# Kernel optimization log

Hardware: AMD Instinct MI355X
Metric: run time of the kernel (lower is better)

The kernel has to match this reference:

```python
import jax, jax.numpy as jnp
import numpy as np

H = 16        # attention heads
KVH = 4       # kv heads (GQA)
D = 128       # qk head_dim = qk_nope(64) + qk_rope(64)
ROPE = 64     # rotary sub-dim
VCH = 128     # v_channels
HID = 2048    # hidden size
E = 8         # routed experts
K = 2         # top-k
EPS = 1e-6
THETA = 10000.0


def rmsnorm(x, w):
    return x * jax.lax.rsqrt(jnp.mean(x * x, axis=-1, keepdims=True) + EPS) * w


def apply_rope(x, pos):
    # x: [T, h, ROPE]; rotate-half convention on the rope sub-dim
    half = ROPE // 2
    inv_freq = 1.0 / (THETA ** (jnp.arange(half, dtype=jnp.float32) / half))
    ang = pos.astype(jnp.float32)[:, None] * inv_freq          # [T, half]
    cos = jnp.cos(ang)[:, None, :]
    sin = jnp.sin(ang)[:, None, :]
    x1, x2 = x[..., :half], x[..., half:]
    return jnp.concatenate([x1 * cos - x2 * sin, x1 * sin + x2 * cos], axis=-1)


def swiglu(x, w_gate, w_up, w_down):
    return (jax.nn.silu(x @ w_gate) * (x @ w_up)) @ w_down


def setup_inputs() -> dict:
    key = jax.random.key(0)
    ks = jax.random.split(key, 16)
    T = 2048
    sc = 0.02
    n = lambda k, s: jax.random.normal(k, s, dtype=jnp.float32) * sc
    return {
        "x": jax.random.normal(ks[0], (T, HID), dtype=jnp.float32),
        "positions": jnp.arange(T, dtype=jnp.int32),
        "ln1_w": jnp.ones((HID,), jnp.float32),
        "qkv_w": n(ks[1], (HID, H * D + KVH * D + KVH * VCH)),
        "qkv_b": n(ks[2], (H * D + KVH * D + KVH * VCH,)),
        "k_ln_w": jnp.ones((D,), jnp.float32),
        "o_w": n(ks[3], (H * VCH, HID)),
        "ln2_w": jnp.ones((HID,), jnp.float32),
        "router_w": n(ks[4], (HID, E)),
        "w1": n(ks[5], (E, HID, 512)),
        "w2": n(ks[6], (E, 512, HID)),
        "w3": n(ks[7], (E, HID, 512)),
        "sw1": n(ks[8], (HID, 1024)),
        "sw2": n(ks[9], (1024, HID)),
        "sw3": n(ks[10], (HID, 1024)),
    }


def reference(x, positions, ln1_w, qkv_w, qkv_b, k_ln_w, o_w, ln2_w,
              router_w, w1, w2, w3, sw1, sw2, sw3):
    T = x.shape[0]
    # --- attention block ---
    h = rmsnorm(x, ln1_w)
    qkv = h @ qkv_w + qkv_b
    q = qkv[:, : H * D].reshape(T, H, D)
    k = qkv[:, H * D : H * D + KVH * D].reshape(T, KVH, D)
    v = qkv[:, H * D + KVH * D :].reshape(T, KVH, VCH)
    k = rmsnorm(k, k_ln_w)  # per-head k_layernorm over head_dim
    # rope applied to the trailing qk_rope_dim of q/k
    q = jnp.concatenate([q[..., : D - ROPE], apply_rope(q[..., D - ROPE :], positions)], -1)
    k = jnp.concatenate([k[..., : D - ROPE], apply_rope(k[..., D - ROPE :], positions)], -1)
    rep = H // KVH
    kf = jnp.repeat(k, rep, axis=1)   # [T, H, D]
    vf = jnp.repeat(v, rep, axis=1)   # [T, H, VCH]
    scale = D ** -0.5
    scores = jnp.einsum("qhd,khd->hqk", q, kf) * scale
    causal = jnp.tril(jnp.ones((T, T), dtype=bool))
    scores = jnp.where(causal[None], scores, jnp.float32(-1e30))
    p = jax.nn.softmax(scores, axis=-1)
    attn = jnp.einsum("hqk,khv->qhv", p, vf).reshape(T, H * VCH)
    x = x + attn @ o_w
    # --- MoE block: shared expert + top-k routed experts ---
    h2 = rmsnorm(x, ln2_w)
    probs = jax.nn.softmax(h2 @ router_w, axis=-1)            # [T, E]
    topw, topi = jax.lax.top_k(probs, K)
    topw = topw / jnp.sum(topw, axis=-1, keepdims=True)        # renormalize top-k
    combine = jnp.sum(jax.nn.one_hot(topi, E, dtype=h2.dtype) * topw[..., None], axis=1)  # [T, E]
    moe = swiglu(h2, sw1, sw3, sw2)                            # shared expert
    for e in range(E):  # small fixed expert count
        moe = moe + combine[:, e : e + 1] * swiglu(h2, w1[e], w3[e], w2[e])
    return x + moe
```

## Files before the change

### kernel.cpp

```cpp
#include <hip/hip_runtime.h>


typedef _Float16 half_t;
typedef _Float16 half8 __attribute__((ext_vector_type(8)));
typedef _Float16 half2v __attribute__((ext_vector_type(2)));
typedef float    f32x4 __attribute__((ext_vector_type(4)));
typedef float    floatx4 __attribute__((ext_vector_type(4)));

#define T_TOK 2048
#define HIDN  2048
#define NH    16
#define NKVH  4
#define HD    128
#define QKV_N 3072
#define NEXP  8
#define NPAIR_MAX 4608

#define MFMA16(a,b,c) __builtin_amdgcn_mfma_f32_16x16x32_f16(a,b,c,0,0,0)

__device__ __forceinline__ void gload_lds16(const half_t* g, half_t* l) {
    __builtin_amdgcn_global_load_lds(
        (const __attribute__((address_space(1))) void*)g,
        (__attribute__((address_space(3))) void*)l, 16, 0, 0);
}

__device__ __forceinline__ float silu_f(float g) {
    return g / (1.0f + expf(-g));
}

__global__ __launch_bounds__(256)
void rmsnorm_split_k(const float* __restrict__ x, const float* __restrict__ w,
                     half_t* __restrict__ hi, half_t* __restrict__ lo)
{
    const int row = blockIdx.x, tid = threadIdx.x;
    const float* xr = x + (size_t)row * HIDN;
    floatx4 v0 = *(const floatx4*)(xr + tid * 8);
    floatx4 v1 = *(const floatx4*)(xr + tid * 8 + 4);
    float ss = v0[0]*v0[0] + v0[1]*v0[1] + v0[2]*v0[2] + v0[3]*v0[3]
             + v1[0]*v1[0] + v1[1]*v1[1] + v1[2]*v1[2] + v1[3]*v1[3];
    for (int o = 32; o; o >>= 1) ss += __shfl_down(ss, o);
    __shared__ float red[4];
    if ((tid & 63) == 0) red[tid >> 6] = ss;
    __syncthreads();
    ss = red[0] + red[1] + red[2] + red[3];
    float rs = rsqrtf(ss * (1.0f / HIDN) + 1e-6f);
    floatx4 w0 = *(const floatx4*)(w + tid * 8);
    floatx4 w1 = *(const floatx4*)(w + tid * 8 + 4);
    float vv[8] = { v0[0]*w0[0], v0[1]*w0[1], v0[2]*w0[2], v0[3]*w0[3],
                    v1[0]*w1[0], v1[1]*w1[1], v1[2]*w1[2], v1[3]*w1[3] };
    half8 hv, lv;
#pragma unroll
    for (int j = 0; j < 8; ++j) {
        float o = vv[j] * rs;
        half_t h = (half_t)o;
        hv[j] = h;
        lv[j] = (half_t)((o - (float)h) * 1024.0f);
    }
    *(half8*)(hi + (size_t)row * HIDN + tid * 8) = hv;
    if (lo) *(half8*)(lo + (size_t)row * HIDN + tid * 8) = lv;
}

__global__ __launch_bounds__(256)
void transpose_split2(const float* __restrict__ src,
                      half_t* __restrict__ dh, half_t* __restrict__ dl,
                      int sstride, int dstride)
{
    __shared__ float tile[32][36];
    const int n0 = blockIdx.x * 32, k0 = blockIdx.y * 32;
    const int tid = threadIdx.x;
    {
        int r = tid >> 3, c = (tid & 7) * 4;
        *(floatx4*)&tile[r][c] =
            *(const floatx4*)(src + (size_t)(k0 + r) * sstride + n0 + c);
    }
    __syncthreads();
    int n = tid & 31, g = tid >> 5, gg = g & 3;
    half8 hv;
    if (g < 4) {
#pragma unroll
        for (int j = 0; j < 8; ++j) hv[j] = (half_t)tile[gg * 8 + j][n];
        *(half8*)(dh + (size_t)(n0 + n) * dstride + k0 + gg * 8) = hv;
    } else {
#pragma unroll
        for (int j = 0; j < 8; ++j) {
            float v = tile[gg * 8 + j][n];
            half_t h = (half_t)v;
            hv[j] = (half_t)((v - (float)h) * 1024.0f);
        }
        *(half8*)(dl + (size_t)(n0 + n) * dstride + k0 + gg * 8) = hv;
    }
}

__global__ __launch_bounds__(256)
void transpose_f16(const float* __restrict__ src, half_t* __restrict__ dh,
                   int sstride, int dstride)
{
    __shared__ float tile[32][68];
    const int n0 = blockIdx.x * 64, k0 = blockIdx.y * 32;
    const int tid = threadIdx.x;
    {
        int r = tid >> 3, c = (tid & 7) * 4;
        const float* s = src + (size_t)(k0 + r) * sstride + n0;
        *(floatx4*)&tile[r][c]      = *(const floatx4*)(s + c);
        *(floatx4*)&tile[r][c + 32] = *(const floatx4*)(s + c + 32);
    }
    __syncthreads();
    int n = tid & 63, g = tid >> 6;
    half8 hv;
#pragma unroll
    for (int j = 0; j < 8; ++j) hv[j] = (half_t)tile[g * 8 + j][n];
    *(half8*)(dh + (size_t)(n0 + n) * dstride + k0 + g * 8) = hv;
}

__global__ __launch_bounds__(256)
void vt_transpose_perm(const float* __restrict__ src, half_t* __restrict__ dh)
{
    __shared__ float tile[32][68];
    const int n0 = blockIdx.x * 64, k0 = blockIdx.y * 32;
    const int tid = threadIdx.x;
    {
        int r = tid >> 3, c = (tid & 7) * 4;
        const float* s = src + (size_t)(k0 + r) * QKV_N + n0;
        *(floatx4*)&tile[r][c]      = *(const floatx4*)(s + c);
        *(floatx4*)&tile[r][c + 32] = *(const floatx4*)(s + c + 32);
    }
    __syncthreads();
    int n = tid & 63, g = tid >> 6;
    half8 hv;
#pragma unroll
    for (int tt = 0; tt < 8; ++tt) {
        int c_src = (tt & 1) * 16 + 4 * g + (tt >> 1);
        hv[tt] = (half_t)tile[c_src][n];
    }
    *(half8*)(dh + (size_t)(n0 + n) * T_TOK + k0 + g * 8) = hv;
}

__global__ __launch_bounds__(256)
void w13_transpose(const float* __restrict__ sw1, const float* __restrict__ w1,
                   const float* __restrict__ sw3, const float* __restrict__ w3,
                   half_t* __restrict__ dst)
{
    __shared__ float tile[32][68];
    const int n0 = blockIdx.x * 64, k0 = blockIdx.y * 32;
    const int tid = threadIdx.x;
    const float* base;
    int stride;
    if (n0 < 1024)      { base = sw1 + n0; stride = 1024; }
    else if (n0 < 2048) { base = sw3 + (n0 - 1024); stride = 1024; }
    else if (n0 < 6144) { int e = (n0 - 2048) >> 9;
                          base = w1 + (size_t)e * HIDN * 512 + ((n0 - 2048) & 511);
                          stride = 512; }
    else                { int e = (n0 - 6144) >> 9;
                          base = w3 + (size_t)e * HIDN * 512 + ((n0 - 6144) & 511);
                          stride = 512; }
    {
        int r = tid >> 3, c = (tid & 7) * 4;
        const float* s = base + (size_t)(k0 + r) * stride;
        *(floatx4*)&tile[r][c]      = *(const floatx4*)(s + c);
        *(floatx4*)&tile[r][c + 32] = *(const floatx4*)(s + c + 32);
    }
    __syncthreads();
    int n = tid & 63, g = tid >> 6;
    half8 hv;
#pragma unroll
    for (int j = 0; j < 8; ++j) hv[j] = (half_t)tile[g * 8 + j][n];
    *(half8*)(dst + (size_t)(n0 + n) * HIDN + k0 + g * 8) = hv;
}

__global__ __launch_bounds__(256)
void w2_transpose(const float* __restrict__ sw2, const float* __restrict__ w2,
                  half_t* __restrict__ dst)
{
    __shared__ float tile[32][68];
    const int n0 = blockIdx.x * 64, k0 = blockIdx.y * 32;
    const int tid = threadIdx.x;
    {
        int r = tid >> 3, c = (tid & 7) * 4;
        int k = k0 + r;
        const float* s;
        if (k < 1024) s = sw2 + (size_t)k * HIDN + n0;
        else {
            int e = (k - 1024) >> 9, kk = (k - 1024) & 511;
            s = w2 + ((size_t)e * 512 + kk) * HIDN + n0;
        }
        *(floatx4*)&tile[r][c]      = *(const floatx4*)(s + c);
        *(floatx4*)&tile[r][c + 32] = *(const floatx4*)(s + c + 32);
    }
    __syncthreads();
    int n = tid & 63, g = tid >> 6;
    half8 hv;
#pragma unroll
    for (int j = 0; j < 8; ++j) hv[j] = (half_t)tile[g * 8 + j][n];
    *(half8*)(dst + (size_t)(n0 + n) * 5120 + k0 + g * 8) = hv;
}

__global__ __launch_bounds__(256)
void owu_kernel(const float* __restrict__ ow, const float* __restrict__ ln2w,
                const float* __restrict__ rw, float* __restrict__ owu,
                int* __restrict__ cnt, int* __restrict__ pairTok,
                float* __restrict__ pairW)
{
    if (blockIdx.x < 18) {
        int idx = blockIdx.x * 256 + threadIdx.x;
        if (idx < NPAIR_MAX) { pairTok[idx] = 0; pairW[idx] = 0.0f; }
        if (idx < NEXP) cnt[idx] = 0;
    }
    const int k = blockIdx.x * 4 + (threadIdx.x >> 6);
    const int lane = threadIdx.x & 63;
    float acc[NEXP] = {};
    const float* row = ow + (size_t)k * HIDN;
#pragma unroll
    for (int j = 0; j < 8; ++j) {
        int c = j * 256 + lane * 4;
        floatx4 ov = *(const floatx4*)(row + c);
        floatx4 lw = *(const floatx4*)(ln2w + c);
#pragma unroll
        for (int i = 0; i < 4; ++i) {
            float s = ov[i] * lw[i];
            const float* rwc = rw + (size_t)(c + i) * NEXP;
#pragma unroll
            for (int e = 0; e < NEXP; ++e) acc[e] += s * rwc[e];
        }
    }
#pragma unroll
    for (int e = 0; e < NEXP; ++e)
        for (int o = 32; o; o >>= 1) acc[e] += __shfl_down(acc[e], o);
    if (lane == 0) {
#pragma unroll
        for (int e = 0; e < NEXP; ++e) owu[(size_t)k * NEXP + e] = acc[e];
    }
}

__global__ __launch_bounds__(256)
void z_kernel(const float* __restrict__ qkv, const float* __restrict__ owu,
              float* __restrict__ zbuf)
{
    const int kv = blockIdx.x, tid = threadIdx.x;
    const int hh = tid >> 4, li = tid & 15;
    const float* vrow = qkv + (size_t)kv * QKV_N + 2560 + (hh >> 2) * HD;
    const int d0 = li * 8;
    float acc[NEXP] = {};
#pragma unroll
    for (int j = 0; j < 8; ++j) {
        float v = vrow[d0 + j];
        const float* ou = owu + (size_t)(hh * HD + d0 + j) * NEXP;
#pragma unroll
        for (int e = 0; e < NEXP; ++e) acc[e] += v * ou[e];
    }
#pragma unroll
    for (int e = 0; e < NEXP; ++e)
        for (int o = 1; o < 16; o <<= 1) acc[e] += __shfl_xor(acc[e], o);
    if (li == 0) {
#pragma unroll
        for (int e = 0; e < NEXP; ++e)
            zbuf[((size_t)hh * T_TOK + kv) * NEXP + e] = acc[e];
    }
}

template<bool SPLIT, int BM>
__global__ __launch_bounds__(256, 2)
void gemm_f16(const half_t* __restrict__ Ah, const half_t* __restrict__ Al,
              const half_t* __restrict__ Bth, const half_t* __restrict__ Btl,
              const float* __restrict__ bias, const float* __restrict__ res,
              float* __restrict__ Cf, half_t* __restrict__ Ch,
              int M, int N, int K, int lda, int ldb)
{
    constexpr int NBUF = SPLIT ? 2 : 1;
    constexpr int MR = BM / 32;
    __shared__ half_t As[2][NBUF][BM * 32];
    __shared__ half_t Bs[2][NBUF][128 * 32];
    const int tid = threadIdx.x, lane = tid & 63, wid = tid >> 6;
    const int l15 = lane & 15, l4 = lane >> 4;
    const int row0 = blockIdx.y * BM, col0 = blockIdx.x * 128;
    const int wr = (wid >> 1) * (BM / 2), wc = (wid & 1) * 64;
    f32x4 accM[MR][4] = {}, accC[MR][4] = {};
    const int lrw = lane >> 2, lcl = (lane & 3) * 8;

#define STAGE(BUF, K0)                                                        \
    do {                                                                      \
        _Pragma("unroll")                                                     \
        for (int j = 0; j < BM / 64; ++j) {                                   \
            const int r = wid * (BM / 4) + j * 16;                            \
            const size_t ga = (size_t)(row0 + r + lrw) * lda + (K0) + lcl;    \
            gload_lds16(Ah + ga, &As[BUF][0][r * 32]);                        \
            if constexpr (SPLIT) gload_lds16(Al + ga, &As[BUF][1][r * 32]);   \
        }                                                                     \
        _Pragma("unroll")                                                     \
        for (int j = 0; j < 2; ++j) {                                         \
            const int r = wid * 32 + j * 16;                                  \
            const size_t gb = (size_t)(col0 + r + lrw) * ldb + (K0) + lcl;    \
            gload_lds16(Bth + gb, &Bs[BUF][0][r * 32]);                       \
            if constexpr (SPLIT) gload_lds16(Btl + gb, &Bs[BUF][1][r * 32]);  \
        }                                                                     \
    } while (0)

    STAGE(0, 0);
    __syncthreads();
    int cur = 0;
    for (int k0 = 0; k0 < K; k0 += 32, cur ^= 1) {
        if (k0 + 32 < K) STAGE(cur ^ 1, k0 + 32);
        half8 ah[MR], al[MR], bh[4], bl[4];
#pragma unroll
        for (int m = 0; m < MR; ++m) {
            int off = (wr + m * 16 + l15) * 32 + l4 * 8;
            ah[m] = *(const half8*)&As[cur][0][off];
            if constexpr (SPLIT) al[m] = *(const half8*)&As[cur][1][off];
        }
#pragma unroll
        for (int n = 0; n < 4; ++n) {
            int off = (wc + n * 16 + l15) * 32 + l4 * 8;
            bh[n] = *(const half8*)&Bs[cur][0][off];
            if constexpr (SPLIT) bl[n] = *(const half8*)&Bs[cur][1][off];
        }
#pragma unroll
        for (int m = 0; m < MR; ++m)
#pragma unroll
            for (int n = 0; n < 4; ++n) {
                accM[m][n] = MFMA16(ah[m], bh[n], accM[m][n]);
                if constexpr (SPLIT) {
                    accC[m][n] = MFMA16(ah[m], bl[n], accC[m][n]);
                    accC[m][n] = MFMA16(al[m], bh[n], accC[m][n]);
                }
            }
        __syncthreads();
    }
#undef STAGE

#pragma unroll
    for (int m = 0; m < MR; ++m) {
#pragma unroll
        for (int n = 0; n < 4; ++n) {
            int gr0 = row0 + wr + m * 16 + l4 * 4;
            int gc  = col0 + wc + n * 16 + l15;
            float b = bias ? bias[gc] : 0.0f;
#pragma unroll
            for (int i = 0; i < 4; ++i) {
                float v = accM[m][n][i];
                if constexpr (SPLIT) v += accC[m][n][i] * (1.0f / 1024.0f);
                v += b;
                size_t idx = (size_t)(gr0 + i) * N + gc;
                if (res) v += res[idx];
                if (Cf) Cf[idx] = v;
                if (Ch) Ch[idx] = (half_t)v;
            }
        }
    }
}

__global__ __launch_bounds__(256, 2)
void gemm_gu_all(const half_t* __restrict__ h2, const half_t* __restrict__ W13t,
                 const int* __restrict__ pairTok, const int* __restrict__ basep,
                 const float* __restrict__ pairW,
                 half_t* __restrict__ As_out, half_t* __restrict__ Ab_out)
{
    __shared__ half_t As[2][64 * 32];
    __shared__ half_t Bs[2][128 * 32];
    __shared__ half_t ex[64][136];
    const int bid = blockIdx.x;
    const bool grouped = (bid >= 512);
    int ct, row0;
    if (!grouped) { ct = bid & 15;          row0 = (bid >> 4) * 64; }
    else          { int g = bid - 512; ct = g & 7; row0 = (g >> 3) * 64; }
    const int tid = threadIdx.x, lane = tid & 63, wid = tid >> 6;
    const int l15 = lane & 15, l4 = lane >> 4;
    const int lrw = lane >> 2, lcl = (lane & 3) * 8;
    int gbase, ubase;
    if (grouped) {
        int e = 0;
#pragma unroll
        for (int i = 1; i < NEXP; ++i) if (row0 >= basep[i]) e = i;
        gbase = 2048 + 512 * e + ct * 64;
        ubase = 6144 + 512 * e + ct * 64;
    } else {
        gbase = ct * 64;
        ubase = 1024 + ct * 64;
    }
    const int wr = (wid >> 1) * 32, wc = (wid & 1) * 64;
    const half_t* Abase;
    if (grouped) {
        const int tok = pairTok[row0 + wid * 16 + lrw];
        Abase = h2 + (size_t)tok * HIDN + lcl;
    } else {
        Abase = h2 + (size_t)(row0 + wid * 16 + lrw) * HIDN + lcl;
    }
    f32x4 acc[2][4] = {};

#define GSTAGE(BUF, K0)                                                       \
    do {                                                                      \
        gload_lds16(Abase + (K0), &As[BUF][(wid * 16) * 32]);                 \
        _Pragma("unroll")                                                     \
        for (int j = 0; j < 2; ++j) {                                         \
            const int r = wid * 32 + j * 16;                                  \
            const int grow = (r < 64) ? gbase + r : ubase + (r - 64);         \
            const size_t gb = (size_t)(grow + lrw) * HIDN + (K0) + lcl;       \
            gload_lds16(W13t + gb, &Bs[BUF][r * 32]);                         \
        }                                                                     \
    } while (0)

    GSTAGE(0, 0);
    __syncthreads();
    int cur = 0;
    for (int k0 = 0; k0 < HIDN; k0 += 32, cur ^= 1) {
        if (k0 + 32 < HIDN) GSTAGE(cur ^ 1, k0 + 32);
        half8 ah[2], bh[4];
#pragma unroll
        for (int m = 0; m < 2; ++m)
            ah[m] = *(const half8*)&As[cur][(wr + m * 16 + l15) * 32 + l4 * 8];
#pragma unroll
        for (int n = 0; n < 4; ++n)
            bh[n] = *(const half8*)&Bs[cur][(wc + n * 16 + l15) * 32 + l4 * 8];
#pragma unroll
        for (int m = 0; m < 2; ++m)
#pragma unroll
            for (int n = 0; n < 4; ++n)
                acc[m][n] = MFMA16(ah[m], bh[n], acc[m][n]);
        __syncthreads();
    }
#undef GSTAGE

#pragma unroll
    for (int m = 0; m < 2; ++m)
#pragma unroll
        for (int n = 0; n < 4; ++n)
#pragma unroll
            for (int i = 0; i < 4; ++i)
                ex[wr + m * 16 + l4 * 4 + i][wc + n * 16 + l15] =
                    (half_t)acc[m][n][i];
    __syncthreads();
    const int OSTR = grouped ? 512 : 1024;
    half_t* outp = grouped ? Ab_out : As_out;
#pragma unroll
    for (int w2 = 0; w2 < 2; ++w2) {
        int unit = tid * 2 + w2;
        int row = unit >> 3, cgx = (unit & 7) * 8;
        half8 g8 = *(const half8*)&ex[row][cgx];
        half8 u8 = *(const half8*)&ex[row][64 + cgx];
        float wgt = grouped ? pairW[row0 + row] : 1.0f;
        half8 o8;
#pragma unroll
        for (int j = 0; j < 8; ++j)
            o8[j] = (half_t)(silu_f((float)g8[j]) * (float)u8[j] * wgt);
        *(half8*)(outp + (size_t)(row0 + row) * OSTR + ct * 64 + cgx) = o8;
    }
}

__global__ __launch_bounds__(256, 2)
void gemm_down_all(const half_t* __restrict__ As_sh, const half_t* __restrict__ Ab,
                   const half_t* __restrict__ W2t, const int* __restrict__ basep,
                   const float* __restrict__ x2, float* __restrict__ out,
                   half_t* __restrict__ Ypair)
{
    __shared__ half_t Asm[2][64 * 32];
    __shared__ half_t Bsm[2][128 * 32];
    const int tid = threadIdx.x, lane = tid & 63, wid = tid >> 6;
    const int l15 = lane & 15, l4 = lane >> 4;
    const int lrw = lane >> 2, lcl = (lane & 3) * 8;
    const int col0 = blockIdx.x * 128;
    const bool shared = (blockIdx.y < 32);
    const int row0 = (shared ? blockIdx.y : blockIdx.y - 32) * 64;
    const half_t* A;
    int lda, K, bcol;
    if (shared) { A = As_sh; lda = 1024; K = 1024; bcol = 0; }
    else {
        int e = 0;
#pragma unroll
        for (int i = 1; i < NEXP; ++i) if (row0 >= basep[i]) e = i;
        A = Ab; lda = 512; K = 512; bcol = 1024 + 512 * e;
    }
    const int wr = (wid >> 1) * 32, wc = (wid & 1) * 64;
    f32x4 acc[2][4] = {};

#define DSTAGE(BUF, K0)                                                       \
    do {                                                                      \
        const size_t ga = (size_t)(row0 + wid * 16 + lrw) * lda + (K0) + lcl; \
        gload_lds16(A + ga, &Asm[BUF][(wid * 16) * 32]);                      \
        _Pragma("unroll")                                                     \
        for (int j = 0; j < 2; ++j) {                                         \
            const int r = wid * 32 + j * 16;                                  \
            const size_t gb = (size_t)(col0 + r + lrw) * 5120 + bcol + (K0) + lcl; \
            gload_lds16(W2t + gb, &Bsm[BUF][r * 32]);                         \
        }                                                                     \
    } while (0)

    DSTAGE(0, 0);
    __syncthreads();
    int cur = 0;
    for (int k0 = 0; k0 < K; k0 += 32, cur ^= 1) {
        if (k0 + 32 < K) DSTAGE(cur ^ 1, k0 + 32);
        half8 ah[2], bh[4];
#pragma unroll
        for (int m = 0; m < 2; ++m)
            ah[m] = *(const half8*)&Asm[cur][(wr + m * 16 + l15) * 32 + l4 * 8];
#pragma unroll
        for (int n = 0; n < 4; ++n)
            bh[n] = *(const half8*)&Bsm[cur][(wc + n * 16 + l15) * 32 + l4 * 8];
#pragma unroll
        for (int m = 0; m < 2; ++m)
#pragma unroll
            for (int n = 0; n < 4; ++n)
                acc[m][n] = MFMA16(ah[m], bh[n], acc[m][n]);
        __syncthreads();
    }
#undef DSTAGE

#pragma unroll
    for (int m = 0; m < 2; ++m)
#pragma unroll
        for (int n = 0; n < 4; ++n) {
            int gr0 = row0 + wr + m * 16 + l4 * 4;
            int gc  = col0 + wc + n * 16 + l15;
#pragma unroll
            for (int i = 0; i < 4; ++i) {
                size_t idx = (size_t)(gr0 + i) * HIDN + gc;
                if (shared) out[idx] = x2[idx] + acc[m][n][i];
                else        Ypair[idx] = (half_t)acc[m][n][i];
            }
        }
}

__global__ __launch_bounds__(256)
void qkv_prep(const float* __restrict__ qkv, const int* __restrict__ pos,
              const float* __restrict__ klnw,
              half_t* __restrict__ qh, half_t* __restrict__ ql,
              half_t* __restrict__ kh, half_t* __restrict__ kl)
{
    const int t = blockIdx.x, tid = threadIdx.x, lane = tid & 63, wid = tid >> 6;
    const float* row = qkv + (size_t)t * QKV_N;
    __shared__ float cs[32], sn[32];
    if (tid < 32) {
        double freq = exp((double)tid * -0.28782313662425572);
        double ang = (double)pos[t] * freq;
        const double twopi = 6.283185307179586476925286766559;
        ang -= twopi * floor(ang * (1.0 / twopi));
        float a = (float)ang;
        cs[tid] = cosf(a);
        sn[tid] = sinf(a);
    }
    __syncthreads();

    const float qscale = 0.08838834764831845f;
    {
        const int hh = tid >> 4, d0 = (tid & 15) * 8;
        const float* qrow = row + hh * HD;
        float outv[8];
        if (d0 < 64) {
#pragma unroll
            for (int j = 0; j < 8; ++j) outv[j] = qrow[d0 + j];
        } else if (d0 < 96) {
            int j0 = d0 - 64;
#pragma unroll
            for (int j = 0; j < 8; ++j) {
                int jj = j0 + j;
                outv[j] = qrow[64 + jj] * cs[jj] - qrow[96 + jj] * sn[jj];
            }
        } else {
            int j0 = d0 - 96;
#pragma unroll
            for (int j = 0; j < 8; ++j) {
                int jj = j0 + j;
                outv[j] = qrow[64 + jj] * sn[jj] + qrow[96 + jj] * cs[jj];
            }
        }
        half8 hv, lv;
#pragma unroll
        for (int j = 0; j < 8; ++j) {
            float o = outv[j] * qscale;
            half_t h = (half_t)o;
            hv[j] = h;
            lv[j] = (half_t)((o - (float)h) * 1024.0f);
        }
        size_t base = (size_t)t * (NH * HD) + hh * HD + d0;
        *(half8*)(qh + base) = hv;
        *(half8*)(ql + base) = lv;
    }
    {
        const float* krow = row + NH * HD + wid * HD;
        float a0 = krow[lane], a1 = krow[64 + lane];
        float ss = a0 * a0 + a1 * a1;
        for (int o = 32; o; o >>= 1) ss += __shfl_down(ss, o);
        ss = __shfl(ss, 0);
        float rs = rsqrtf(ss * (1.0f / HD) + 1e-6f);
        float n0 = a0 * rs * klnw[lane];
        float n1 = a1 * rs * klnw[64 + lane];
        float other = __shfl_xor(n1, 32);
        int j = lane & 31;
        float o1 = (lane < 32) ? (n1 * cs[j] - other * sn[j])
                               : (other * sn[j] + n1 * cs[j]);
        size_t base = (size_t)t * (NKVH * HD) + wid * HD;
        half_t h;
        h = (half_t)n0; kh[base + lane] = h;
        kl[base + lane] = (half_t)((n0 - (float)h) * 1024.0f);
        h = (half_t)o1; kh[base + 64 + lane] = h;
        kl[base + 64 + lane] = (half_t)((o1 - (float)h) * 1024.0f);
    }
}

__global__ __launch_bounds__(256, 2)
void attn_kernel(const half_t* __restrict__ qh, const half_t* __restrict__ ql,
                 const half_t* __restrict__ kh, const half_t* __restrict__ kl,
                 const half_t* __restrict__ vth, const float* __restrict__ zbuf,
                 half_t* __restrict__ oh,
                 float* __restrict__ Op0, float* __restrict__ Op1,
                 float* __restrict__ Op2, float* __restrict__ ml,
                 float* __restrict__ zpart, float* __restrict__ zfin)
{
    const int bid = blockIdx.x;
    const int h = bid & 15;
    int rrem = bid >> 4, q = 31, nch = 6, c = 0;
    for (; q >= 0; --q) {
        nch = (q + 6) / 6;
        if (rrem < nch) { c = rrem; break; }
        rrem -= nch;
    }
    const int nt = q + 1;
    const int kvbeg = ((c * nt) / nch) * 64;
    const int kvend = (((c + 1) * nt) / nch) * 64;

    const int kvh = h >> 2;
    const int tid = threadIdx.x, lane = tid & 63, wid = tid >> 6;
    const int q0 = q * 64 + wid * 16;
    const int l15 = lane & 15, l4 = lane >> 4;

    __shared__ half_t Ksh[64][136], Ksl[64][136];
    __shared__ half_t Vsh[128][72];
    __shared__ half_t Ph[4][16][72];
    __shared__ float  zsh[64][8];

    half8 qfh[4], qfl[4];
    {
        const size_t qb = (size_t)(q0 + l15) * (NH * HD) + h * HD + l4 * 8;
#pragma unroll
        for (int cc = 0; cc < 4; ++cc) {
            qfh[cc] = *(const half8*)(qh + qb + cc * 32);
            qfl[cc] = *(const half8*)(ql + qb + cc * 32);
        }
    }

    f32x4 om[8] = {};
    f32x4 zacA[4] = {}, zacB[4] = {};
    float mrow[4] = { -1e30f, -1e30f, -1e30f, -1e30f };
    float lrow[4] = {};

    const int kr = tid >> 2, kc0 = (tid & 3) * 32;
    const int vd = tid >> 1, vc0 = (tid & 1) * 32;
    const int zr = tid >> 3, zc = tid & 7;
    uint4 rkh0, rkh1, rkh2, rkh3, rkl0, rkl1, rkl2, rkl3;
    uint4 rv0, rv1, rv2, rv3;
    float rz0, rz1;

#define LOAD_TILE(KV0)                                                        \
    do {                                                                      \
        size_t sk = (size_t)((KV0) + kr) * (NKVH * HD) + kvh * HD + kc0;      \
        rkh0 = *(const uint4*)(kh + sk);       rkl0 = *(const uint4*)(kl + sk);      \
        rkh1 = *(const uint4*)(kh + sk + 8);   rkl1 = *(const uint4*)(kl + sk + 8);  \
        rkh2 = *(const uint4*)(kh + sk + 16);  rkl2 = *(const uint4*)(kl + sk + 16); \
        rkh3 = *(const uint4*)(kh + sk + 24);  rkl3 = *(const uint4*)(kl + sk + 24); \
        size_t sv = (size_t)(kvh * HD + vd) * T_TOK + (KV0) + vc0;            \
        rv0 = *(const uint4*)(vth + sv);       rv1 = *(const uint4*)(vth + sv + 8);  \
        rv2 = *(const uint4*)(vth + sv + 16);  rv3 = *(const uint4*)(vth + sv + 24); \
        rz0 = zbuf[((size_t)h * T_TOK + (KV0) + zr) * 8 + zc];                \
        rz1 = zbuf[((size_t)h * T_TOK + (KV0) + 32 + zr) * 8 + zc];           \
    } while (0)

    LOAD_TILE(kvbeg);
    for (int kv0 = kvbeg; kv0 < kvend; kv0 += 64) {
        *(uint4*)&Ksh[kr][kc0]      = rkh0;  *(uint4*)&Ksl[kr][kc0]      = rkl0;
        *(uint4*)&Ksh[kr][kc0 + 8]  = rkh1;  *(uint4*)&Ksl[kr][kc0 + 8]  = rkl1;
        *(uint4*)&Ksh[kr][kc0 + 16] = rkh2;  *(uint4*)&Ksl[kr][kc0 + 16] = rkl2;
        *(uint4*)&Ksh[kr][kc0 + 24] = rkh3;  *(uint4*)&Ksl[kr][kc0 + 24] = rkl3;
        *(uint4*)&Vsh[vd][vc0]      = rv0;   *(uint4*)&Vsh[vd][vc0 + 8]  = rv1;
        *(uint4*)&Vsh[vd][vc0 + 16] = rv2;   *(uint4*)&Vsh[vd][vc0 + 24] = rv3;
        zsh[zr][zc]      = rz0;
        zsh[32 + zr][zc] = rz1;
        __syncthreads();
        if (kv0 + 64 < kvend) LOAD_TILE(kv0 + 64);

        f32x4 sf[4];
        __builtin_amdgcn_s_setprio(1);
#pragma unroll
        for (int t2 = 0; t2 < 4; ++t2) {
            f32x4 s = {}, sc1 = {}, sc2 = {};
#pragma unroll
            for (int cc = 0; cc < 4; ++cc) {
                half8 bh = *(const half8*)&Ksh[t2 * 16 + l15][cc * 32 + l4 * 8];
                half8 bl = *(const half8*)&Ksl[t2 * 16 + l15][cc * 32 + l4 * 8];
                s   = MFMA16(qfh[cc], bh, s);
                sc1 = MFMA16(qfh[cc], bl, sc1);
                sc2 = MFMA16(qfl[cc], bh, sc2);
            }
            sf[t2] = s + (sc1 + sc2) * (1.0f / 1024.0f);
        }
        __builtin_amdgcn_s_setprio(0);

        float pmax[4];
#pragma unroll
        for (int i = 0; i < 4; ++i) {
            const int qg = q0 + l4 * 4 + i;
#pragma unroll
            for (int t2 = 0; t2 < 4; ++t2) {
                int kvg = kv0 + t2 * 16 + l15;
                if (kvg > qg) sf[t2][i] = -1e30f;
            }
            float mx = fmaxf(fmaxf(sf[0][i], sf[1][i]),
                             fmaxf(sf[2][i], sf[3][i]));
#pragma unroll
            for (int o = 1; o < 16; o <<= 1) mx = fmaxf(mx, __shfl_xor(mx, o));
            pmax[i] = mx;
        }
        float dm = fmaxf(fmaxf(pmax[0] - mrow[0], pmax[1] - mrow[1]),
                         fmaxf(pmax[2] - mrow[2], pmax[3] - mrow[3]));
        if (__any(dm > 6.0f)) {
#pragma unroll
            for (int i = 0; i < 4; ++i) {
                float mnew = fmaxf(mrow[i], pmax[i]);
                float resc = expf(mrow[i] - mnew);
                lrow[i] *= resc;
                zacA[i] *= resc;  zacB[i] *= resc;
#pragma unroll
                for (int c8 = 0; c8 < 8; ++c8) om[c8][i] *= resc;
                mrow[i] = mnew;
            }
        }
        f32x4 zt0a = *(const f32x4*)&zsh[l15][0];
        f32x4 zt0b = *(const f32x4*)&zsh[l15][4];
        f32x4 zt1a = *(const f32x4*)&zsh[16 + l15][0];
        f32x4 zt1b = *(const f32x4*)&zsh[16 + l15][4];
        f32x4 zt2a = *(const f32x4*)&zsh[32 + l15][0];
        f32x4 zt2b = *(const f32x4*)&zsh[32 + l15][4];
        f32x4 zt3a = *(const f32x4*)&zsh[48 + l15][0];
        f32x4 zt3b = *(const f32x4*)&zsh[48 + l15][4];
#pragma unroll
        for (int i = 0; i < 4; ++i) {
            float p0 = expf(sf[0][i] - mrow[i]);
            float p1 = expf(sf[1][i] - mrow[i]);
            float p2 = expf(sf[2][i] - mrow[i]);
            float p3 = expf(sf[3][i] - mrow[i]);
            lrow[i] += (p0 + p1) + (p2 + p3);
            zacA[i] += p0 * zt0a + p1 * zt1a + p2 * zt2a + p3 * zt3a;
            zacB[i] += p0 * zt0b + p1 * zt1b + p2 * zt2b + p3 * zt3b;
            half2v ppA = { (half_t)p0, (half_t)p1 };
            half2v ppB = { (half_t)p2, (half_t)p3 };
            *(half2v*)&Ph[wid][l4 * 4 + i][l15 * 2]      = ppA;
            *(half2v*)&Ph[wid][l4 * 4 + i][32 + l15 * 2] = ppB;
        }

        half8 pa0 = *(const half8*)&Ph[wid][l15][l4 * 8];
        half8 pa1 = *(const half8*)&Ph[wid][l15][32 + l4 * 8];
        __builtin_amdgcn_s_setprio(1);
#pragma unroll
        for (int c8 = 0; c8 < 8; ++c8) {
            half8 v0 = *(const half8*)&Vsh[c8 * 16 + l15][l4 * 8];
            half8 v1 = *(const half8*)&Vsh[c8 * 16 + l15][32 + l4 * 8];
            om[c8] = MFMA16(pa0, v0, om[c8]);
            om[c8] = MFMA16(pa1, v1, om[c8]);
        }
        __builtin_amdgcn_s_setprio(0);
        __syncthreads();
    }
#undef LOAD_TILE

#pragma unroll
    for (int i = 0; i < 4; ++i)
#pragma unroll
        for (int o = 1; o < 16; o <<= 1) lrow[i] += __shfl_xor(lrow[i], o);

    for (int o = 1; o < 16; o <<= 1) {
#pragma unroll
        for (int i = 0; i < 4; ++i)
#pragma unroll
            for (int k = 0; k < 4; ++k) {
                zacA[i][k] += __shfl_xor(zacA[i][k], o);
                zacB[i][k] += __shfl_xor(zacB[i][k], o);
            }
    }
    if (l15 == 0) {
#pragma unroll
        for (int i = 0; i < 4; ++i) {
            int row64 = wid * 16 + l4 * 4 + i;
            if (nch == 1) {
                float invl = 1.0f / lrow[i];
                size_t zo = ((size_t)(q * 64 + row64) * 16 + h) * 8;
                *(f32x4*)&zfin[zo]     = zacA[i] * invl;
                *(f32x4*)&zfin[zo + 4] = zacB[i] * invl;
            } else {
                size_t zo = ((size_t)bid * 64 + row64) * 8;
                *(f32x4*)&zpart[zo]     = zacA[i];
                *(f32x4*)&zpart[zo + 4] = zacB[i];
            }
        }
    }

    if (nch == 1) {
#pragma unroll
        for (int c8 = 0; c8 < 8; ++c8) {
#pragma unroll
            for (int i = 0; i < 4; ++i) {
                float v = om[c8][i] / lrow[i];
                size_t idx = (size_t)(q0 + l4 * 4 + i) * (NH * HD) + h * HD
                           + c8 * 16 + l15;
                oh[idx] = (half_t)v;
            }
        }
    } else {
        float* Op = (bid < 768)  ? Op0 + (size_t)bid * 8192
                  : (bid < 1280) ? Op1 + (size_t)(bid - 768) * 8192
                                 : Op2 + (size_t)(bid - 1280) * 8192;
#pragma unroll
        for (int c8 = 0; c8 < 8; ++c8) {
#pragma unroll
            for (int i = 0; i < 4; ++i) {
                int row64 = wid * 16 + l4 * 4 + i;
                Op[row64 * 128 + c8 * 16 + l15] = om[c8][i];
            }
        }
        if (l15 == 0) {
#pragma unroll
            for (int i = 0; i < 4; ++i) {
                int row64 = wid * 16 + l4 * 4 + i;
                ml[(size_t)bid * 128 + row64]      = mrow[i];
                ml[(size_t)bid * 128 + 64 + row64] = lrow[i];
            }
        }
    }
}

__device__ __forceinline__ const float* slot_ptr(int s, const float* Op0,
                                                 const float* Op1,
                                                 const float* Op2)
{
    return (s < 768)  ? Op0 + (size_t)s * 8192
         : (s < 1280) ? Op1 + (size_t)(s - 768) * 8192
                      : Op2 + (size_t)(s - 1280) * 8192;
}

__global__ __launch_bounds__(256)
void attn_combine(const float* __restrict__ Op0, const float* __restrict__ Op1,
                  const float* __restrict__ Op2, const float* __restrict__ ml,
                  const float* __restrict__ zpart,
                  half_t* __restrict__ oh, float* __restrict__ zfin)
{
    const int bid = blockIdx.x;
    const int h = bid & 15, q = 6 + (bid >> 4);
    const int nch = (q + 6) / 6;
    int r0 = 0;
    for (int j = 31; j > q; --j) r0 += (j + 6) / 6;
    const int tid = threadIdx.x;
    const int row = tid >> 2, cg = (tid & 3) * 32;

    float M = -1e30f;
    for (int c = 0; c < nch; ++c) {
        int s = (r0 + c) * 16 + h;
        M = fmaxf(M, ml[(size_t)s * 128 + row]);
    }
    float wsum = 0.0f;
    for (int c = 0; c < nch; ++c) {
        int s = (r0 + c) * 16 + h;
        wsum += ml[(size_t)s * 128 + 64 + row] *
                expf(ml[(size_t)s * 128 + row] - M);
    }
    float inv = 1.0f / wsum;

    if ((tid & 3) == 0) {
        f32x4 a = {0,0,0,0}, b = {0,0,0,0};
        for (int c = 0; c < nch; ++c) {
            int s = (r0 + c) * 16 + h;
            float w = expf(ml[(size_t)s * 128 + row] - M) * inv;
            size_t zo = ((size_t)s * 64 + row) * 8;
            a += w * (*(const f32x4*)&zpart[zo]);
            b += w * (*(const f32x4*)&zpart[zo + 4]);
        }
        size_t zo = ((size_t)(q * 64 + row) * 16 + h) * 8;
        *(f32x4*)&zfin[zo]     = a;
        *(f32x4*)&zfin[zo + 4] = b;
    }

    size_t obase = (size_t)(q * 64 + row) * (NH * HD) + h * HD + cg;
#pragma unroll
    for (int jj = 0; jj < 4; ++jj) {
        floatx4 a0 = {0,0,0,0}, a1 = {0,0,0,0};
        for (int c = 0; c < nch; ++c) {
            int s = (r0 + c) * 16 + h;
            float w = expf(ml[(size_t)s * 128 + row] - M) * inv;
            const float* base = slot_ptr(s, Op0, Op1, Op2) + row * 128 + cg;
            a0 += w * (*(const floatx4*)(base + jj * 8));
            a1 += w * (*(const floatx4*)(base + jj * 8 + 4));
        }
        half8 hv;
#pragma unroll
        for (int k = 0; k < 4; ++k) {
            hv[k]     = (half_t)a0[k];
            hv[4 + k] = (half_t)a1[k];
        }
        *(half8*)(oh + obase + jj * 8) = hv;
    }
}

__global__ __launch_bounds__(256)
void router_linear(const float* __restrict__ x, const float* __restrict__ zfin,
                   const float* __restrict__ x2,
                   const float* __restrict__ ln2w, const float* __restrict__ rw,
                   int* __restrict__ topi, float* __restrict__ topv,
                   int* __restrict__ cnt, half_t* __restrict__ h2)
{
    const int t = blockIdx.x, tid = threadIdx.x;
    const float* xr2 = x2 + (size_t)t * HIDN + tid * 8;
    floatx4 x2a = *(const floatx4*)(xr2);
    floatx4 x2b = *(const floatx4*)(xr2 + 4);
    float ss = x2a[0]*x2a[0] + x2a[1]*x2a[1] + x2a[2]*x2a[2] + x2a[3]*x2a[3]
             + x2b[0]*x2b[0] + x2b[1]*x2b[1] + x2b[2]*x2b[2] + x2b[3]*x2b[3];
    for (int o = 32; o; o >>= 1) ss += __shfl_down(ss, o);
    __shared__ float red[4];
    if ((tid & 63) == 0) red[tid >> 6] = ss;
    __syncthreads();
    ss = red[0] + red[1] + red[2] + red[3];
    float rs = rsqrtf(ss * (1.0f / HIDN) + 1e-6f);

    const float* xr = x + (size_t)t * HIDN + tid * 8;
    floatx4 xa = *(const floatx4*)(xr);
    floatx4 xb = *(const floatx4*)(xr + 4);
    floatx4 lwa = *(const floatx4*)(ln2w + tid * 8);
    floatx4 lwb = *(const floatx4*)(ln2w + tid * 8 + 4);

    float acc[NEXP] = {};
#pragma unroll
    for (int j = 0; j < 8; ++j) {
        int c = tid * 8 + j;
        float xv = (j < 4 ? xa[j] : xb[j - 4]) * (j < 4 ? lwa[j] : lwb[j - 4]);
        const float* rwc = rw + (size_t)c * NEXP;
#pragma unroll
        for (int e = 0; e < NEXP; ++e) acc[e] += xv * rwc[e];
    }
#pragma unroll
    for (int e = 0; e < NEXP; ++e)
        for (int o = 32; o; o >>= 1) acc[e] += __shfl_down(acc[e], o);
    __shared__ float red8[4][NEXP];
    if ((tid & 63) == 0)
#pragma unroll
        for (int e = 0; e < NEXP; ++e) red8[tid >> 6][e] = acc[e];

    __shared__ float zred[NEXP * 16];
    if (tid < 128) {
        int hh = tid >> 3, e = tid & 7;
        zred[e * 16 + hh] = zfin[((size_t)t * 16 + hh) * 8 + e];
    }

    half8 h2v;
#pragma unroll
    for (int j = 0; j < 8; ++j) {
        float xv = (j < 4 ? x2a[j] : x2b[j - 4]) * (j < 4 ? lwa[j] : lwb[j - 4]);
        h2v[j] = (half_t)(xv * rs);
    }
    *(half8*)(h2 + (size_t)t * HIDN + tid * 8) = h2v;

    __syncthreads();
    if (tid == 0) {
        float lg[NEXP];
#pragma unroll
        for (int e = 0; e < NEXP; ++e) {
            float zs = 0.0f;
#pragma unroll
            for (int hh = 0; hh < 16; ++hh) zs += zred[e * 16 + hh];
            lg[e] = (red8[0][e] + red8[1][e] + red8[2][e] + red8[3][e] + zs) * rs;
        }
        int i1 = 0;
        for (int e = 1; e < NEXP; ++e) if (lg[e] > lg[i1]) i1 = e;
        int i2 = (i1 == 0) ? 1 : 0;
        for (int e = 0; e < NEXP; ++e) if (e != i1 && lg[e] > lg[i2]) i2 = e;
        float mx = lg[i1];
        float p1 = expf(lg[i1] - mx), p2 = expf(lg[i2] - mx);
        float inv = 1.0f / (p1 + p2);
        topi[2 * t] = i1;       topi[2 * t + 1] = i2;
        topv[2 * t] = p1 * inv; topv[2 * t + 1] = p2 * inv;
        atomicAdd(&cnt[i1], 1);
        atomicAdd(&cnt[i2], 1);
    }
}

__global__ __launch_bounds__(256)
void moe_build(const int* __restrict__ cnt, int* __restrict__ basep,
               const int* __restrict__ topi, const float* __restrict__ topv,
               int* __restrict__ pairTok, float* __restrict__ pairW,
               int* __restrict__ pairPos)
{
    const int e = blockIdx.x;
    int base = 0;
    for (int i = 0; i < e; ++i) base += (cnt[i] + 63) & ~63;
    if (threadIdx.x == 0) basep[e] = base;

    const int tid = threadIdx.x, lane = tid & 63, wv = tid >> 6;
    __shared__ int wsum[4];
    int run = base;
    for (int i0 = 0; i0 < 2 * T_TOK; i0 += 256) {
        int i = i0 + tid;
        bool m = (topi[i] == e);
        unsigned long long bal = __ballot(m);
        int lpre = __popcll(bal & ((1ull << lane) - 1ull));
        if (lane == 0) wsum[wv] = (int)__popcll(bal);
        __syncthreads();
        int woff = 0;
        for (int w = 0; w < wv; ++w) woff += wsum[w];
        if (m) {
            int pos = run + woff + lpre;
            pairTok[pos] = i >> 1;
            pairW[pos]   = topv[i];
            pairPos[i]   = pos;
        }
        run += wsum[0] + wsum[1] + wsum[2] + wsum[3];
        __syncthreads();
    }
}

__global__ __launch_bounds__(256)
void moe_final(const half_t* __restrict__ Ypair, const int* __restrict__ pairPos,
               float* __restrict__ out)
{
    int t = blockIdx.x, c0 = threadIdx.x * 8;
    int p1 = pairPos[2 * t], p2 = pairPos[2 * t + 1];
    half8 y1 = *(const half8*)(Ypair + (size_t)p1 * HIDN + c0);
    half8 y2 = *(const half8*)(Ypair + (size_t)p2 * HIDN + c0);
    float* o = out + (size_t)t * HIDN + c0;
    floatx4 a = *(floatx4*)o, b = *(floatx4*)(o + 4);
#pragma unroll
    for (int j = 0; j < 4; ++j) {
        a[j] += (float)y1[j] + (float)y2[j];
        b[j] += (float)y1[4 + j] + (float)y2[4 + j];
    }
    *(floatx4*)o = a;
    *(floatx4*)(o + 4) = b;
}

extern "C" void kernel_launch(void* const* d_in, const int* in_sizes, int n_in,
                              void* d_out, int out_size, void* d_ws, size_t ws_size,
                              hipStream_t stream)
{
    (void)in_sizes; (void)n_in; (void)out_size; (void)ws_size;
    const float* x    = (const float*)d_in[0];
    const int*   pos  = (const int*)  d_in[1];
    const float* ln1w = (const float*)d_in[2];
    const float* qkvw = (const float*)d_in[3];
    const float* qkvb = (const float*)d_in[4];
    const float* klnw = (const float*)d_in[5];
    const float* ow   = (const float*)d_in[6];
    const float* ln2w = (const float*)d_in[7];
    const float* rw   = (const float*)d_in[8];
    const float* w1   = (const float*)d_in[9];
    const float* w2   = (const float*)d_in[10];
    const float* w3   = (const float*)d_in[11];
    const float* sw1  = (const float*)d_in[12];
    const float* sw2  = (const float*)d_in[13];
    const float* sw3  = (const float*)d_in[14];
    float* out = (float*)d_out;

    char* ws = (char*)d_ws;
    const size_t AB = 16842752;
    float*  x2      = (float*)(ws);
    half_t* h_hi    = (half_t*)(ws + AB);
    half_t* h_lo    = (half_t*)(ws + AB + 8388608);
    half_t* qkvwt_h = (half_t*)(ws + AB + 16777216);
    half_t* qkvwt_l = (half_t*)(ws + AB + 29360128);
    float*  qkv     = (float*)(ws + AB + 41943040);
    half_t* q_h     = (half_t*)(ws + AB + 67108864);
    half_t* q_l     = (half_t*)(ws + AB + 75497472);
    half_t* k_h     = (half_t*)(ws + AB + 83886080);
    half_t* k_l     = (half_t*)(ws + AB + 85983232);
    half_t* vt_h    = (half_t*)(ws + AB + 88080384);
    half_t* attn_h  = (half_t*)(ws + AB);
    float*  zbuf    = (float*)(ws + AB + 8388608);
    half_t* owt     = (half_t*)(ws + AB + 16777216);
    float*  ow_u    = (float*)(ws + AB + 25165824);
    float*  mlpart  = (float*)(ws + AB + 25231360);
    float*  Opart0  = (float*)(ws + AB + 41943040);
    float*  Opart1  = (float*)(ws);
    float*  Opart2  = (float*)(ws + AB + 29360128);
    half_t* h2      = (half_t*)(ws + AB + 33554432);
    half_t* W13t    = (half_t*)(ws + AB + 41943040);
    half_t* As_sh   = (half_t*)(ws + AB);
    half_t* Ab      = (half_t*)(ws + AB + 16777216);
    half_t* W2t     = (half_t*)(ws + AB + 41943040);
    half_t* Ypair   = (half_t*)(ws + AB + 92274688);

    char* meta = ws + (size_t)(AB + 117440512);
    int*    cnt     = (int*)  (meta + 0);
    int*    basep   = (int*)  (meta + 128);
    int*    topi    = (int*)  (meta + 256);
    float*  topv    = (float*)(meta + 16640);
    int*    pairPos = (int*)  (meta + 33024);
    int*    pairTok = (int*)  (meta + 49408);
    float*  pairW   = (float*)(meta + 67840);
    float*  zpart   = (float*)(meta + 131072);
    float*  zfin    = (float*)(meta + 131072 + 3342336);

    dim3 b256(256);

    rmsnorm_split_k<<<T_TOK, b256, 0, stream>>>(x, ln1w, h_hi, h_lo);
    transpose_split2<<<dim3(QKV_N / 32, HIDN / 32), b256, 0, stream>>>(
        qkvw, qkvwt_h, qkvwt_l, QKV_N, HIDN);
    gemm_f16<true, 64><<<dim3(QKV_N / 128, T_TOK / 64), b256, 0, stream>>>(
        h_hi, h_lo, qkvwt_h, qkvwt_l, qkvb, nullptr, qkv, nullptr,
        T_TOK, QKV_N, HIDN, HIDN, HIDN);
    qkv_prep<<<T_TOK, b256, 0, stream>>>(qkv, pos, klnw, q_h, q_l, k_h, k_l);
    vt_transpose_perm<<<dim3(512 / 64, T_TOK / 32), b256, 0, stream>>>(
        qkv + 2560, vt_h);
    transpose_f16<<<dim3(HIDN / 64, HIDN / 32), b256, 0, stream>>>(
        ow, owt, HIDN, HIDN);
    owu_kernel<<<512, b256, 0, stream>>>(ow, ln2w, rw, ow_u,
                                         cnt, pairTok, pairW);
    z_kernel<<<T_TOK, b256, 0, stream>>>(qkv, ow_u, zbuf);
    attn_kernel<<<1632, b256, 0, stream>>>(
        q_h, q_l, k_h, k_l, vt_h, zbuf, attn_h,
        Opart0, Opart1, Opart2, mlpart, zpart, zfin);
    attn_combine<<<416, b256, 0, stream>>>(Opart0, Opart1, Opart2, mlpart,
                                           zpart, attn_h, zfin);
    gemm_f16<false, 64><<<dim3(HIDN / 128, T_TOK / 64), b256, 0, stream>>>(
        attn_h, nullptr, owt, nullptr, nullptr, x, x2, nullptr,
        T_TOK, HIDN, HIDN, HIDN, HIDN);
    router_linear<<<T_TOK, b256, 0, stream>>>(
        x, zfin, x2, ln2w, rw, topi, topv, cnt, h2);
    moe_build<<<NEXP, b256, 0, stream>>>(cnt, basep, topi, topv,
                                         pairTok, pairW, pairPos);
    w13_transpose<<<dim3(10240 / 64, HIDN / 32), b256, 0, stream>>>(
        sw1, w1, sw3, w3, W13t);
    gemm_gu_all<<<512 + 8 * (NPAIR_MAX / 64), b256, 0, stream>>>(
        h2, W13t, pairTok, basep, pairW, As_sh, Ab);
    w2_transpose<<<dim3(HIDN / 64, 5120 / 32), b256, 0, stream>>>(sw2, w2, W2t);
    gemm_down_all<<<dim3(16, 104), b256, 0, stream>>>(
        As_sh, Ab, W2t, basep, x2, out, Ypair);
    moe_final<<<T_TOK, b256, 0, stream>>>(Ypair, pairPos, out);
}
```

Baseline: 614.2 us.

## Fold router z-accumulation into the PV MFMA as a ninth value tile

The per-head router projection z (8 experts) used to be accumulated in the attention kernel with scalar FMAs on fp32 values plus a cross-lane shuffle reduction. Now z is stored transposed and in fp16, in a permuted layout matching the P·V operand. It is appended to the V shared tile as 16 extra rows so one more MFMA per kv tile produces it. This removes the VALU accumulation and the shuffle reduction, at the cost of fp16 precision for z and of P also being fp16 in that product, which may affect router logits and top-k selection.

```diff
diff --git a/kernel.cpp b/kernel.cpp
--- a/kernel.cpp
+++ b/kernel.cpp
@@ -233,7 +233,7 @@
 
 __global__ __launch_bounds__(256)
 void z_kernel(const float* __restrict__ qkv, const float* __restrict__ owu,
-              float* __restrict__ zbuf)
+              half_t* __restrict__ zt)
 {
     const int kv = blockIdx.x, tid = threadIdx.x;
     const int hh = tid >> 4, li = tid & 15;
@@ -251,9 +251,12 @@
     for (int e = 0; e < NEXP; ++e)
         for (int o = 1; o < 16; o <<= 1) acc[e] += __shfl_xor(acc[e], o);
     if (li == 0) {
+        int j = kv & 31;
+        int s = ((j & 15) << 1) | (j >> 4);
+        size_t base = (size_t)(kv & ~31) + s;
 #pragma unroll
         for (int e = 0; e < NEXP; ++e)
-            zbuf[((size_t)hh * T_TOK + kv) * NEXP + e] = acc[e];
+            zt[(size_t)(hh * 8 + e) * T_TOK + base] = (half_t)acc[e];
     }
 }
 
@@ -598,7 +601,7 @@
 __global__ __launch_bounds__(256, 2)
 void attn_kernel(const half_t* __restrict__ qh, const half_t* __restrict__ ql,
                  const half_t* __restrict__ kh, const half_t* __restrict__ kl,
-                 const half_t* __restrict__ vth, const float* __restrict__ zbuf,
+                 const half_t* __restrict__ vth, const half_t* __restrict__ zt,
                  half_t* __restrict__ oh,
                  float* __restrict__ Op0, float* __restrict__ Op1,
                  float* __restrict__ Op2, float* __restrict__ ml,
@@ -622,9 +625,8 @@
     const int l15 = lane & 15, l4 = lane >> 4;
 
     __shared__ half_t Ksh[64][136], Ksl[64][136];
-    __shared__ half_t Vsh[128][72];
+    __shared__ half_t Vsh[144][72];
     __shared__ half_t Ph[4][16][72];
-    __shared__ float  zsh[64][8];
 
     half8 qfh[4], qfl[4];
     {
@@ -636,17 +638,16 @@
         }
     }
 
-    f32x4 om[8] = {};
-    f32x4 zacA[4] = {}, zacB[4] = {};
+    f32x4 om[9] = {};
     float mrow[4] = { -1e30f, -1e30f, -1e30f, -1e30f };
     float lrow[4] = {};
 
     const int kr = tid >> 2, kc0 = (tid & 3) * 32;
     const int vd = tid >> 1, vc0 = (tid & 1) * 32;
-    const int zr = tid >> 3, zc = tid & 7;
+    const int ze = tid >> 5, zc0 = (tid & 31) * 2;
     uint4 rkh0, rkh1, rkh2, rkh3, rkl0, rkl1, rkl2, rkl3;
     uint4 rv0, rv1, rv2, rv3;
-    float rz0, rz1;
+    unsigned rzw;
 
 #define LOAD_TILE(KV0)                                                        \
     do {                                                                      \
@@ -658,8 +659,7 @@
         size_t sv = (size_t)(kvh * HD + vd) * T_TOK + (KV0) + vc0;            \
         rv0 = *(const uint4*)(vth + sv);       rv1 = *(const uint4*)(vth + sv + 8);  \
         rv2 = *(const uint4*)(vth + sv + 16);  rv3 = *(const uint4*)(vth + sv + 24); \
-        rz0 = zbuf[((size_t)h * T_TOK + (KV0) + zr) * 8 + zc];                \
-        rz1 = zbuf[((size_t)h * T_TOK + (KV0) + 32 + zr) * 8 + zc];           \
+        rzw = *(const unsigned*)(zt + (size_t)(h * 8 + ze) * T_TOK + (KV0) + zc0);   \
     } while (0)
 
     LOAD_TILE(kvbeg);
@@ -670,8 +670,7 @@
         *(uint4*)&Ksh[kr][kc0 + 24] = rkh3;  *(uint4*)&Ksl[kr][kc0 + 24] = rkl3;
         *(uint4*)&Vsh[vd][vc0]      = rv0;   *(uint4*)&Vsh[vd][vc0 + 8]  = rv1;
         *(uint4*)&Vsh[vd][vc0 + 16] = rv2;   *(uint4*)&Vsh[vd][vc0 + 24] = rv3;
-        zsh[zr][zc]      = rz0;
-        zsh[32 + zr][zc] = rz1;
+        *(unsigned*)&Vsh[128 + ze][zc0] = rzw;
         __syncthreads();
         if (kv0 + 64 < kvend) LOAD_TILE(kv0 + 64);
 
@@ -715,20 +714,11 @@
                 float mnew = fmaxf(mrow[i], pmax[i]);
                 float resc = expf(mrow[i] - mnew);
                 lrow[i] *= resc;
-                zacA[i] *= resc;  zacB[i] *= resc;
-#pragma unroll
-                for (int c8 = 0; c8 < 8; ++c8) om[c8][i] *= resc;
+#pragma unroll
+                for (int c8 = 0; c8 < 9; ++c8) om[c8][i] *= resc;
                 mrow[i] = mnew;
             }
         }
-        f32x4 zt0a = *(const f32x4*)&zsh[l15][0];
-        f32x4 zt0b = *(const f32x4*)&zsh[l15][4];
-        f32x4 zt1a = *(const f32x4*)&zsh[16 + l15][0];
-        f32x4 zt1b = *(const f32x4*)&zsh[16 + l15][4];
-        f32x4 zt2a = *(const f32x4*)&zsh[32 + l15][0];
-        f32x4 zt2b = *(const f32x4*)&zsh[32 + l15][4];
-        f32x4 zt3a = *(const f32x4*)&zsh[48 + l15][0];
-        f32x4 zt3b = *(const f32x4*)&zsh[48 + l15][4];
 #pragma unroll
         for (int i = 0; i < 4; ++i) {
             float p0 = expf(sf[0][i] - mrow[i]);
@@ -736,8 +726,6 @@
             float p2 = expf(sf[2][i] - mrow[i]);
             float p3 = expf(sf[3][i] - mrow[i]);
             lrow[i] += (p0 + p1) + (p2 + p3);
-            zacA[i] += p0 * zt0a + p1 * zt1a + p2 * zt2a + p3 * zt3a;
-            zacB[i] += p0 * zt0b + p1 * zt1b + p2 * zt2b + p3 * zt3b;
             half2v ppA = { (half_t)p0, (half_t)p1 };
             half2v ppB = { (half_t)p2, (half_t)p3 };
             *(half2v*)&Ph[wid][l4 * 4 + i][l15 * 2]      = ppA;
@@ -748,7 +736,7 @@
         half8 pa1 = *(const half8*)&Ph[wid][l15][32 + l4 * 8];
         __builtin_amdgcn_s_setprio(1);
 #pragma unroll
-        for (int c8 = 0; c8 < 8; ++c8) {
+        for (int c8 = 0; c8 < 9; ++c8) {
             half8 v0 = *(const half8*)&Vsh[c8 * 16 + l15][l4 * 8];
             half8 v1 = *(const half8*)&Vsh[c8 * 16 + l15][32 + l4 * 8];
             om[c8] = MFMA16(pa0, v0, om[c8]);
@@ -764,28 +752,16 @@
 #pragma unroll
         for (int o = 1; o < 16; o <<= 1) lrow[i] += __shfl_xor(lrow[i], o);
 
-    for (int o = 1; o < 16; o <<= 1) {
-#pragma unroll
-        for (int i = 0; i < 4; ++i)
-#pragma unroll
-            for (int k = 0; k < 4; ++k) {
-                zacA[i][k] += __shfl_xor(zacA[i][k], o);
-                zacB[i][k] += __shfl_xor(zacB[i][k], o);
-            }
-    }
-    if (l15 == 0) {
+    if (l15 < 8) {
+        const int e = l15;
 #pragma unroll
         for (int i = 0; i < 4; ++i) {
             int row64 = wid * 16 + l4 * 4 + i;
             if (nch == 1) {
-                float invl = 1.0f / lrow[i];
-                size_t zo = ((size_t)(q * 64 + row64) * 16 + h) * 8;
-                *(f32x4*)&zfin[zo]     = zacA[i] * invl;
-                *(f32x4*)&zfin[zo + 4] = zacB[i] * invl;
+                zfin[((size_t)(q * 64 + row64) * 16 + h) * 8 + e] =
+                    om[8][i] / lrow[i];
             } else {
-                size_t zo = ((size_t)bid * 64 + row64) * 8;
-                *(f32x4*)&zpart[zo]     = zacA[i];
-                *(f32x4*)&zpart[zo + 4] = zacB[i];
+                zpart[((size_t)bid * 64 + row64) * 8 + e] = om[8][i];
             }
         }
     }
@@ -1065,7 +1041,7 @@
     half_t* k_l     = (half_t*)(ws + AB + 85983232);
     half_t* vt_h    = (half_t*)(ws + AB + 88080384);
     half_t* attn_h  = (half_t*)(ws + AB);
-    float*  zbuf    = (float*)(ws + AB + 8388608);
+    half_t* zt      = (half_t*)(ws + AB + 8388608);
     half_t* owt     = (half_t*)(ws + AB + 16777216);
     float*  ow_u    = (float*)(ws + AB + 25165824);
     float*  mlpart  = (float*)(ws + AB + 25231360);
@@ -1105,9 +1081,9 @@
         ow, owt, HIDN, HIDN);
     owu_kernel<<<512, b256, 0, stream>>>(ow, ln2w, rw, ow_u,
                                          cnt, pairTok, pairW);
-    z_kernel<<<T_TOK, b256, 0, stream>>>(qkv, ow_u, zbuf);
+    z_kernel<<<T_TOK, b256, 0, stream>>>(qkv, ow_u, zt);
     attn_kernel<<<1632, b256, 0, stream>>>(
-        q_h, q_l, k_h, k_l, vt_h, zbuf, attn_h,
+        q_h, q_l, k_h, k_l, vt_h, zt, attn_h,
         Opart0, Opart1, Opart2, mlpart, zpart, zfin);
     attn_combine<<<416, b256, 0, stream>>>(Opart0, Opart1, Opart2, mlpart,
                                            zpart, attn_h, zfin);
```

Measured after the change: 601.0 us. -2.1%, faster.
